# Kernel tuning notes

Hardware: AMD Instinct MI355X
Metric: run time of the kernel (lower is better)

Reference implementation:

```python
import jax, jax.numpy as jnp
import numpy as np

_PHI = (1.0 + 5.0 ** 0.5) / 2.0
_VS = np.array([[0, 1, _PHI], [0, 1, -_PHI], [0, -1, _PHI], [0, -1, -_PHI],
                [1, _PHI, 0], [1, -_PHI, 0], [-1, _PHI, 0], [-1, -_PHI, 0],
                [_PHI, 0, 1], [_PHI, 0, -1], [-_PHI, 0, 1], [-_PHI, 0, -1]], dtype=np.float32)
_VS = _VS / np.linalg.norm(_VS, axis=-1, keepdims=True)  # 12 icosahedron vertices
_COLOR_COM = np.array([(0, 1, 2, 3, 4, 5), (0, 5, 4, 3, 2, 1), (2, 5, 4, 1, 0, 3), (5, 0, 1, 3, 2, 4),
                       (3, 5, 2, 0, 4, 1), (4, 0, 5, 2, 1, 3), (1, 3, 4, 2, 0, 5), (1, 0, 2, 4, 3, 5),
                       (4, 1, 2, 5, 0, 3), (3, 1, 4, 0, 2, 5), (5, 1, 0, 4, 2, 3), (2, 4, 5, 3, 0, 1)])
_INV = np.argsort(_COLOR_COM, axis=-1)  # inverse perms: scatter_(-1, color_com, W) == gather with _INV
_C2V = np.array([(0, 1), (6, 7), (2, 11), (4, 9), (5, 8), (3, 10)])
_ROLL = np.array([(0, 1, 2, 3, 4, 5), (0, 2, 3, 4, 5, 1), (0, 3, 4, 5, 1, 2), (0, 4, 5, 1, 2, 3), (0, 5, 1, 2, 3, 4)])
_HEADS = 8


def _build_sym(Wp):
    """(..., 18) raw params -> (..., 13, 12, 6) symmetry-expanded weights."""
    lead = Wp.shape[:-1]
    top = jnp.concatenate([Wp[..., 0:1], jnp.repeat(Wp[..., 1:2], 5, axis=-1)], axis=-1)[..., None, :]
    bot = jnp.concatenate([Wp[..., 2:3], jnp.repeat(Wp[..., 3:4], 5, axis=-1)], axis=-1)[..., None, :]
    cen = jnp.concatenate([Wp[..., 4:5], jnp.repeat(Wp[..., 5:6], 5, axis=-1)], axis=-1)[..., None, :]
    sym = Wp[..., 6:18].reshape(lead + (2, 6))[..., _ROLL].reshape(lead + (10, 6))
    W13 = jnp.concatenate([top, bot, sym, cen], axis=-2)  # (..., 13, 6)
    return W13[..., _INV]  # (..., 13, 12, 6): rotated copies via inverse color permutations


def setup_inputs() -> dict:
    key = jax.random.key(0)
    ks = jax.random.split(key, 6)
    bs, V, n, di, do = 1, 2048, 16, 32, 64
    s = 0.05
    return {
        "neighbor_index": jax.random.randint(ks[0], (bs, V, n), 0, V),
        "vertices": jax.random.normal(ks[1], (bs, V, 3), dtype=jnp.float32),
        "feature_map": jax.random.normal(ks[2], (bs, di, V, 6), dtype=jnp.float32),
        "W_dim": jax.random.normal(ks[3], (di + 1, di), dtype=jnp.float32) * s,
        "W": jax.random.normal(ks[4], (do, di, 18), dtype=jnp.float32) * s,
        "W_dir": jax.random.normal(ks[5], (di * _HEADS, 18), dtype=jnp.float32) * s,
    }


def reference(neighbor_index, vertices, feature_map, W_dim, W, W_dir):
    bs, V, n = neighbor_index.shape
    do, di, _ = W.shape
    H = _HEADS
    dph = di // H
    vs = jnp.asarray(_VS)
    c2v = jnp.asarray(_C2V)
    # neighbor direction (normalized)
    neigh = jax.vmap(lambda v, idx: v[idx])(vertices, neighbor_index)  # (bs,V,n,3)
    nd = neigh - vertices[:, :, None, :]
    ndn = nd / jnp.maximum(jnp.linalg.norm(nd, axis=-1, keepdims=True), 1e-12)
    # symmetry-expanded weights
    W_ro = _build_sym(W)       # (do, di, 13, 12, 6)
    Wd_ro = _build_sym(W_dir)  # (di*H, 13, 12, 6)
    # gather neighbor features: (bs, di, V, n, 6)
    nf = jax.vmap(lambda fm, idx: fm[:, idx])(feature_map, neighbor_index)
    # direction features discretized onto the 6 color axes
    de = jnp.einsum('vi,bqni->bqnv', vs, ndn)          # (bs,V,n,12)
    de = de[..., c2v].max(axis=-1)                      # (bs,V,n,6)
    cross = jnp.concatenate([nf, de[:, None]], axis=1)  # (bs, di+1, V, n, 6)
    cross = jnp.einsum('co,bcpni->bopni', W_dim, cross)  # (bs, di, V, n, 6)
    # per-head attention over neighbors
    Wdr = Wd_ro.reshape(H, di, 13, 12, 6).transpose(0, 1, 2, 4, 3)  # (h, c, k, i, r)
    act = jnp.einsum('hckir,bcpni->hbkpnr', Wdr[:, :, :12], cross) / (dph ** 0.5)
    act = jax.nn.softmax(act, axis=-2)                  # softmax over neighbors n
    cross_h = cross.reshape(bs, H, dph, V, n, 6)
    nfm = jnp.einsum('hbkpnr,bhcpni->bhckpir', act, cross_h).reshape(bs, di, 12, V, 6, 12)
    feat = jnp.einsum('dckri,bckpir->bdkpr', W_ro[:, :, :12], nfm)   # (bs,do,12,V,12)
    center = jnp.einsum('dcri,bcpi->bdpr', W_ro[:, :, 12], feature_map)  # (bs,do,V,12)
    ka = feat.sum(axis=2) + center                       # (bs,do,V,12)
    ka = ka[..., c2v].max(axis=-1)                       # (bs,do,V,6)
    return (ka, feature_map)
```

## Files before the change

### kernel.cpp

```cpp
#include <hip/hip_runtime.h>
#include <cstdint>
#include <cstddef>

#define NN 16
#define DI 32
#define DO 64

typedef short bf16x8 __attribute__((ext_vector_type(8)));
typedef short bf16x4 __attribute__((ext_vector_type(4)));
typedef float f32x4 __attribute__((ext_vector_type(4)));

#if defined(__has_builtin)
#  if __has_builtin(__builtin_amdgcn_mfma_f32_16x16x16_bf16)
#    define MFMA_K16(a, b, c) __builtin_amdgcn_mfma_f32_16x16x16_bf16(a, b, c, 0, 0, 0)
#    define HAVE_K16 1
#  elif __has_builtin(__builtin_amdgcn_mfma_f32_16x16x16bf16_1k)
#    define MFMA_K16(a, b, c) __builtin_amdgcn_mfma_f32_16x16x16bf16_1k(a, b, c, 0, 0, 0)
#    define HAVE_K16 1
#  endif
#endif

__device__ __constant__ int c_INV[12][6] = {
  {0,1,2,3,4,5},{0,5,4,3,2,1},{4,3,0,5,2,1},{1,2,4,3,5,0},
  {3,5,2,0,4,1},{1,4,3,5,0,2},{4,0,3,1,2,5},{1,0,2,4,3,5},
  {4,1,2,5,0,3},{3,1,4,0,2,5},{2,1,4,5,3,0},{4,5,0,3,1,2}};
__device__ __constant__ int c_ROLL[5][6] = {
  {0,1,2,3,4,5},{0,2,3,4,5,1},{0,3,4,5,1,2},{0,4,5,1,2,3},{0,5,1,2,3,4}};
__device__ __constant__ float c_VS[12][3] = {
  {0.f, 0.5257311121f, 0.8506508084f},
  {0.f, 0.5257311121f, -0.8506508084f},
  {0.f, -0.5257311121f, 0.8506508084f},
  {0.f, -0.5257311121f, -0.8506508084f},
  {0.5257311121f, 0.8506508084f, 0.f},
  {0.5257311121f, -0.8506508084f, 0.f},
  {-0.5257311121f, 0.8506508084f, 0.f},
  {-0.5257311121f, -0.8506508084f, 0.f},
  {0.8506508084f, 0.f, 0.5257311121f},
  {0.8506508084f, 0.f, -0.5257311121f},
  {-0.8506508084f, 0.f, 0.5257311121f},
  {-0.8506508084f, 0.f, -0.5257311121f}};
__device__ __constant__ int c_C2V[6][2] = {{0,1},{6,7},{2,11},{4,9},{5,8},{3,10}};

__device__ inline unsigned int bfround(float f) {
  unsigned int u = __float_as_uint(f);
  return u + 0x7fffu + ((u >> 16) & 1u);
}
__device__ inline unsigned int pk2(float a, float b) {
  return __builtin_amdgcn_perm(bfround(b), bfround(a), 0x07060302u);
}
__device__ inline unsigned short f2bf_fast(float a) {
  return (unsigned short)(bfround(a) >> 16);
}
__device__ inline uint4 pack8(const float* v8) {
  uint4 o4;
  o4.x = pk2(v8[0], v8[1]);
  o4.y = pk2(v8[2], v8[3]);
  o4.z = pk2(v8[4], v8[5]);
  o4.w = pk2(v8[6], v8[7]);
  return o4;
}

__device__ inline unsigned int q4i8(f32x4 o) {
  int q0 = (int)rintf(fminf(fmaxf(o[0] * 64.f, -127.f), 127.f));
  int q1 = (int)rintf(fminf(fmaxf(o[1] * 64.f, -127.f), 127.f));
  int q2 = (int)rintf(fminf(fmaxf(o[2] * 64.f, -127.f), 127.f));
  int q3 = (int)rintf(fminf(fmaxf(o[3] * 64.f, -127.f), 127.f));
  return (unsigned int)((q0 & 255) | ((q1 & 255) << 8) | ((q2 & 255) << 16) | (q3 << 24));
}
__device__ inline bf16x8 dec8(uint2 w) {
  float f0 = (float)(int)(signed char)(w.x & 0xffu);
  float f1 = (float)(int)(signed char)((w.x >> 8) & 0xffu);
  float f2 = (float)(int)(signed char)((w.x >> 16) & 0xffu);
  float f3 = (float)((int)w.x >> 24);
  float f4 = (float)(int)(signed char)(w.y & 0xffu);
  float f5 = (float)(int)(signed char)((w.y >> 8) & 0xffu);
  float f6 = (float)(int)(signed char)((w.y >> 16) & 0xffu);
  float f7 = (float)((int)w.y >> 24);
  union { unsigned int u[4]; bf16x8 v8; } o;
  o.u[0] = pk2(f0, f1);
  o.u[1] = pk2(f2, f3);
  o.u[2] = pk2(f4, f5);
  o.u[3] = pk2(f6, f7);
  return o.v8;
}

__global__ __launch_bounds__(256) void k0_expand(
    const float* __restrict__ W, const float* __restrict__ Wdir,
    const float* __restrict__ fm, const float* __restrict__ Wdim,
    unsigned short* __restrict__ A_bf,
    unsigned short* __restrict__ W2k,
    unsigned short* __restrict__ Wck,
    unsigned short* __restrict__ fmTbf,
    unsigned short* __restrict__ wdB,
    float* __restrict__ out_fm, int V) {
  int idx = blockIdx.x * 256 + threadIdx.x;
  int nF = 24 * V;
  if (idx < 267264) {
    const float* wsrc; unsigned short* dst;
    int k, r, ci0; float scale;
    if (idx < 27648) {
      int chunk = idx;
      int rl = chunk & 15, u = chunk >> 4;
      int q = u & 3; u >>= 2;
      int ks = u % 6, rt = u / 6;
      int row = rt * 16 + rl;
      int h = row / 144;
      k = (row / 12) % 12; r = row % 12;
      ci0 = ks * 32 + q * 8;
      wsrc = Wdir + h * 576;
      dst = A_bf + (size_t)chunk * 8;
      scale = 0.5f;
    } else if (idx < 248832) {
      int chunk = idx - 27648;
      int d = chunk & 63, u = chunk >> 6;
      int q = u & 3; u >>= 2;
      int ks = u % 6, kr = u / 6;
      k = kr / 12; r = kr % 12;
      ci0 = ks * 32 + q * 8;
      wsrc = W + d * 576;
      dst = W2k + (size_t)chunk * 8;
      scale = 0.015625f;
    } else {
      int chunk = idx - 248832;
      int d = chunk & 63, u = chunk >> 6;
      int q = u & 3; u >>= 2;
      int ks = u % 6;
      r = u / 6; k = 12;
      ci0 = ks * 32 + q * 8;
      wsrc = W + d * 576;
      dst = Wck + (size_t)chunk * 8;
      scale = 1.0f;
    }
    int c = ci0 / 6, i = ci0 - c * 6;
    float v8[8];
    #pragma unroll
    for (int j = 0; j < 8; ++j) {
      int jj = c_INV[r][i];
      int off;
      if (k == 0)       off = (jj == 0) ? 0 : 1;
      else if (k == 1)  off = (jj == 0) ? 2 : 3;
      else if (k == 12) off = (jj == 0) ? 4 : 5;
      else { int a = (k - 2) / 5, rr = (k - 2) % 5; off = 6 + a * 6 + c_ROLL[rr][jj]; }
      v8[j] = scale * wsrc[c * 18 + off];
      ++i; if (i == 6) { i = 0; ++c; }
    }
    *(uint4*)dst = pack8(v8);
  } else if (idx < 267264 + nF) {
    int chunk = idx - 267264;
    int p = chunk / 24, cc = chunk - p * 24;
    int ci0 = cc * 8;
    int c = ci0 / 6, i = ci0 - c * 6;
    float v8[8];
    #pragma unroll
    for (int j = 0; j < 8; ++j) {
      v8[j] = fm[((size_t)c * V + p) * 6 + i];
      ++i; if (i == 6) { i = 0; ++c; }
    }
    *(uint4*)(fmTbf + (size_t)chunk * 8) = pack8(v8);
  } else if (idx < 267264 + nF + 48 * V) {
    int x4 = idx - (267264 + nF);
    ((float4*)out_fm)[x4] = ((const float4*)fm)[x4];
  } else {
    int e = idx - (267264 + nF + 48 * V);
    if (e < 128) {
      int lane = e & 63, ot = e >> 6;
      float v8[8];
      #pragma unroll
      for (int j = 0; j < 8; ++j) {
        int kk = ((lane >> 4) & 3) * 8 + j;
        int o = ot * 16 + (lane & 15);
        v8[j] = Wdim[kk * 32 + o];
      }
      *(uint4*)(wdB + (size_t)e * 8) = pack8(v8);
    }
  }
}

__global__ __launch_bounds__(256, 4) void k12_main(
    const int* __restrict__ nbi, const float* __restrict__ verts,
    const float* __restrict__ fm, const float* __restrict__ Wdim,
    const unsigned short* __restrict__ wdB,
    const unsigned short* __restrict__ A_bf,
    unsigned char* __restrict__ nfm, int V) {
  __shared__ __align__(16) unsigned short in_bf[2][96][40];
  __shared__ __align__(16) float de_s[2][96];
  __shared__ __align__(16) unsigned short crossL[2][192][20];
  int t = threadIdx.x;
  int w = t >> 6, lane = t & 63;
  int quad = lane >> 4, col = lane & 15;
  int p0 = blockIdx.x * 2;
  int v = w & 1, hf = w >> 1;
  int p = p0 + v;

  for (int i = lane; i < 256; i += 64) {
    int n = i >> 4, c = hf * 16 + (i & 15);
    int nb = nbi[p * 16 + n];
    const float* src = fm + ((size_t)c * V + nb) * 6;
    float2 a  = *(const float2*)(src + 0);
    float2 b  = *(const float2*)(src + 2);
    float2 cd = *(const float2*)(src + 4);
    unsigned short* dst = &in_bf[v][n * 6][c];
    dst[0 * 40] = f2bf_fast(a.x);
    dst[1 * 40] = f2bf_fast(a.y);
    dst[2 * 40] = f2bf_fast(b.x);
    dst[3 * 40] = f2bf_fast(b.y);
    dst[4 * 40] = f2bf_fast(cd.x);
    dst[5 * 40] = f2bf_fast(cd.y);
  }
  if (hf == 0 && lane < 16) {
    int n = lane, nb = nbi[p * 16 + n];
    float px = verts[p * 3 + 0], py = verts[p * 3 + 1], pz = verts[p * 3 + 2];
    float qx = verts[nb * 3 + 0] - px, qy = verts[nb * 3 + 1] - py, qz = verts[nb * 3 + 2] - pz;
    float L = sqrtf(qx * qx + qy * qy + qz * qz);
    float inv = 1.0f / fmaxf(L, 1e-12f);
    qx *= inv; qy *= inv; qz *= inv;
    float de[12];
    #pragma unroll
    for (int vv = 0; vv < 12; ++vv)
      de[vv] = c_VS[vv][0] * qx + c_VS[vv][1] * qy + c_VS[vv][2] * qz;
    #pragma unroll
    for (int j = 0; j < 6; ++j)
      de_s[v][n * 6 + j] = fmaxf(de[c_C2V[j][0]], de[c_C2V[j][1]]);
  }
  __syncthreads();

  {
    int vv = w & 1;
    int mtb = (w >> 1) * 3;
    bf16x8 Bf[2];
    #pragma unroll
    for (int ot = 0; ot < 2; ++ot)
      Bf[ot] = *(const bf16x8*)(wdB + (size_t)(ot * 64 + lane) * 8);
    float wd32[2] = {Wdim[1024 + col], Wdim[1024 + 16 + col]};
    #pragma unroll
    for (int mi = 0; mi < 3; ++mi) {
      int mt = mtb + mi;
      bf16x8 a0 = *(const bf16x8*)&in_bf[vv][mt * 16 + col][quad * 8];
      f32x4 du = *(const f32x4*)&de_s[vv][mt * 16 + quad * 4];
      #pragma unroll
      for (int ot = 0; ot < 2; ++ot) {
        f32x4 acc = (f32x4){0.f, 0.f, 0.f, 0.f};
        acc = __builtin_amdgcn_mfma_f32_16x16x32_bf16(a0, Bf[ot], acc, 0, 0, 0);
        #pragma unroll
        for (int r = 0; r < 4; ++r)
          acc[r] = fmaf(du[r], wd32[ot], acc[r]);
        #pragma unroll
        for (int r = 0; r < 4; ++r) {
          int m = mt * 16 + quad * 4 + r;
          int n = m / 6, i = m - n * 6;
          crossL[vv][(ot * 16 + col) * 6 + i][n] = f2bf_fast(acc[r]);
        }
      }
    }
  }
  __syncthreads();

  bf16x8 Afr[2][6];
  #pragma unroll
  for (int pi = 0; pi < 2; ++pi) {
    #pragma unroll
    for (int ks = 0; ks < 6; ++ks) {
      union { unsigned short s[8]; bf16x8 v8; } u;
      #pragma unroll
      for (int j = 0; j < 8; ++j)
        u.s[j] = crossL[pi][ks * 32 + quad * 8 + j][col];
      Afr[pi][ks] = u.v8;
    }
  }

  bf16x8 wf[6];
  {
    const unsigned short* Abase = A_bf + w * 3072 + quad * 128 + col * 8;
    #pragma unroll
    for (int ks = 0; ks < 6; ++ks) wf[ks] = *(const bf16x8*)(Abase + ks * 512);
  }
  for (int rt = w; rt < 72; rt += 4) {
    int h = rt / 9;
    f32x4 acc[2];
    acc[0] = (f32x4){0.f, 0.f, 0.f, 0.f};
    acc[1] = (f32x4){0.f, 0.f, 0.f, 0.f};
    #pragma unroll
    for (int ks = 0; ks < 6; ++ks) {
      acc[0] = __builtin_amdgcn_mfma_f32_16x16x32_bf16(Afr[0][ks], wf[ks], acc[0], 0, 0, 0);
      acc[1] = __builtin_amdgcn_mfma_f32_16x16x32_bf16(Afr[1][ks], wf[ks], acc[1], 0, 0, 0);
    }
    bf16x8 wfn[6];
    {
      int rtn = min(rt + 4, 71);
      const unsigned short* AbaseN = A_bf + rtn * 3072 + quad * 128 + col * 8;
      #pragma unroll
      for (int ks = 0; ks < 6; ++ks) wfn[ks] = *(const bf16x8*)(AbaseN + ks * 512);
    }
    int row0 = h * 24 + col;
    int row1 = min(h * 24 + 16 + col, 191);
    #pragma unroll
    for (int pi = 0; pi < 2; ++pi) {
      float e0 = __expf(acc[pi][0]), e1 = __expf(acc[pi][1]);
      float e2 = __expf(acc[pi][2]), e3 = __expf(acc[pi][3]);
      float s = (e0 + e1) + (e2 + e3);
      s += __shfl_xor(s, 16);
      s += __shfl_xor(s, 32);
      float inv = __builtin_amdgcn_rcpf(s);
      unsigned int lo = pk2(e0 * inv, e1 * inv);
      unsigned int hi = pk2(e2 * inv, e3 * inv);
      f32x4 o0 = (f32x4){0.f, 0.f, 0.f, 0.f}, o1 = o0;
#ifdef HAVE_K16
      union { uint2 u; bf16x4 v4; } bcvt;
      bcvt.u = make_uint2(lo, hi);
      bf16x4 a0 = *(const bf16x4*)&crossL[pi][row0][quad * 4];
      bf16x4 a1 = *(const bf16x4*)&crossL[pi][row1][quad * 4];
      o0 = MFMA_K16(a0, bcvt.v4, o0);
      o1 = MFMA_K16(a1, bcvt.v4, o1);
#else
      int s0l = quad * 32 + col, s1l = s0l + 16;
      unsigned int b0 = (unsigned int)__shfl((int)lo, s0l);
      unsigned int b1 = (unsigned int)__shfl((int)hi, s0l);
      unsigned int b2 = (unsigned int)__shfl((int)lo, s1l);
      unsigned int b3 = (unsigned int)__shfl((int)hi, s1l);
      bool vq = (quad < 2);
      union { uint4 u; bf16x8 v8; } cvt;
      cvt.u = make_uint4(vq ? b0 : 0u, vq ? b1 : 0u, vq ? b2 : 0u, vq ? b3 : 0u);
      union { unsigned short sv[8]; bf16x8 v8; } ua0, ua1;
      #pragma unroll
      for (int j = 0; j < 8; ++j) {
        int nn = quad * 8 + j;
        ua0.sv[j] = (nn < 16) ? crossL[pi][row0][nn] : (unsigned short)0;
        ua1.sv[j] = (nn < 16) ? crossL[pi][row1][nn] : (unsigned short)0;
      }
      o0 = __builtin_amdgcn_mfma_f32_16x16x32_bf16(ua0.v8, cvt.v8, o0, 0, 0, 0);
      o1 = __builtin_amdgcn_mfma_f32_16x16x32_bf16(ua1.v8, cvt.v8, o1, 0, 0, 0);
#endif
      size_t rowbase = (size_t)blockIdx.x * 55296 + (size_t)(rt * 16 + col) * 48 + pi * 24;
      *(unsigned int*)(nfm + rowbase + quad * 4) = q4i8(o0);
      if (quad < 2)
        *(unsigned int*)(nfm + rowbase + 16 + quad * 4) = q4i8(o1);
    }
    #pragma unroll
    for (int ks = 0; ks < 6; ++ks) wf[ks] = wfn[ks];
  }
}

__global__ __launch_bounds__(512) void k3_feat(
    const unsigned short* __restrict__ W2k,
    const unsigned short* __restrict__ Wck,
    const unsigned short* __restrict__ fmTbf,
    const unsigned char* __restrict__ nfm,
    float* __restrict__ out, int V) {
  __shared__ float red[2][3][16][64];
  int pb = blockIdx.x, j = blockIdx.y;
  int t = threadIdx.x, w = t >> 6, lane = t & 63;
  int rhalf = w >> 2, kw = w & 3;
  int r = c_C2V[j][rhalf];
  int quad = lane >> 4, col = lane & 15;
  int p0 = pb * 16;
  f32x4 acc[4];
  #pragma unroll
  for (int m = 0; m < 4; ++m) acc[m] = (f32x4){0.f, 0.f, 0.f, 0.f};

  int base24[6];
  #pragma unroll
  for (int ks = 0; ks < 6; ++ks) {
    int ci = ks * 32 + quad * 8;
    int hh = ci / 24, oo = ci - hh * 24;
    base24[ks] = hh * 6912 + oo;
  }

  int pA = p0 + col;
  const unsigned char* Bn0 = nfm + (size_t)(pA >> 1) * 55296 + (pA & 1) * 24;
  const unsigned short* Bc0 = fmTbf + (size_t)pA * 192;

  int nkb = (kw == 3) ? 4 : 3;
  for (int i = 0; i < nkb; ++i) {
    int kb = kw * 3 + i;
    const unsigned short* Ab;
    int kr48 = 0;
    if (kb < 12) { Ab = W2k + (size_t)(kb * 12 + r) * 12288; kr48 = (kb * 12 + r) * 48; }
    else         { Ab = Wck + (size_t)r * 12288; }
    const unsigned short* Albase = Ab + quad * 512 + col * 8;
    #pragma unroll
    for (int ks = 0; ks < 6; ++ks) {
      bf16x8 b0;
      if (kb < 12) {
        b0 = dec8(*(const uint2*)(Bn0 + base24[ks] + kr48));
      } else {
        b0 = *(const bf16x8*)(Bc0 + ks * 32 + quad * 8);
      }
      #pragma unroll
      for (int m = 0; m < 4; ++m) {
        bf16x8 a = *(const bf16x8*)(Albase + ks * 2048 + m * 128);
        acc[m] = __builtin_amdgcn_mfma_f32_16x16x32_bf16(a, b0, acc[m], 0, 0, 0);
      }
    }
  }
  if (kw > 0) {
    #pragma unroll
    for (int m = 0; m < 4; ++m)
      #pragma unroll
      for (int rr = 0; rr < 4; ++rr)
        red[rhalf][kw - 1][m * 4 + rr][lane] = acc[m][rr];
  }
  __syncthreads();
  if (kw == 0) {
    #pragma unroll
    for (int m = 0; m < 4; ++m)
      #pragma unroll
      for (int rr = 0; rr < 4; ++rr) {
        int ri = m * 4 + rr;
        acc[m][rr] += red[rhalf][0][ri][lane] + red[rhalf][1][ri][lane] + red[rhalf][2][ri][lane];
      }
  }
  if (w == 4) {
    #pragma unroll
    for (int m = 0; m < 4; ++m)
      #pragma unroll
      for (int rr = 0; rr < 4; ++rr)
        red[1][0][m * 4 + rr][lane] = acc[m][rr];
  }
  __syncthreads();
  if (w == 0) {
    #pragma unroll
    for (int m = 0; m < 4; ++m)
      #pragma unroll
      for (int rr = 0; rr < 4; ++rr) {
        float vmax = fmaxf(acc[m][rr], red[1][0][m * 4 + rr][lane]);
        int d = m * 16 + quad * 4 + rr;
        out[((size_t)d * V + p0 + col) * 6 + j] = vmax;
      }
  }
}

extern "C" void kernel_launch(void* const* d_in, const int* in_sizes, int n_in,
                              void* d_out, int out_size, void* d_ws, size_t ws_size,
                              hipStream_t stream) {
  const int* nbi = (const int*)d_in[0];
  const float* verts = (const float*)d_in[1];
  const float* fm = (const float*)d_in[2];
  const float* Wdim = (const float*)d_in[3];
  const float* W = (const float*)d_in[4];
  const float* Wdir = (const float*)d_in[5];
  float* out = (float*)d_out;
  float* ws = (float*)d_ws;
  int V = in_sizes[0] / NN;

  unsigned short* A_bf  = (unsigned short*)ws;
  unsigned short* W2k   = (unsigned short*)(ws + 110592);
  unsigned short* Wck   = (unsigned short*)(ws + 995328);
  unsigned short* fmTbf = (unsigned short*)(ws + 1069056);
  size_t o = 1069056 + (size_t)96 * V;
  unsigned char* nfm = (unsigned char*)(ws + o);
  o += (size_t)6912 * V;
  unsigned short* wdB = (unsigned short*)(ws + o);

  int n0 = 267392 + 72 * V;
  k0_expand<<<(n0 + 255) / 256, 256, 0, stream>>>(W, Wdir, fm, Wdim, A_bf, W2k, Wck, fmTbf,
                                                  wdB, out + (size_t)DO * V * 6, V);
  k12_main<<<V / 2, 256, 0, stream>>>(nbi, verts, fm, Wdim, wdB, A_bf, nfm, V);
  k3_feat<<<dim3(V / 16, 6), 512, 0, stream>>>(W2k, Wck, fmTbf, nfm, out, V);
}
```

Measured before the change: 153.0 us.

## Split weight expansion and fold k3-only prep into main kernel grid

Result: no change. 150.1 us (-1.9%).

```diff
diff --git a/kernel.cpp b/kernel.cpp
--- a/kernel.cpp
+++ b/kernel.cpp
@@ -84,53 +84,20 @@
   return o.v8;
 }
 
-__global__ __launch_bounds__(256) void k0_expand(
-    const float* __restrict__ W, const float* __restrict__ Wdir,
-    const float* __restrict__ fm, const float* __restrict__ Wdim,
-    unsigned short* __restrict__ A_bf,
-    unsigned short* __restrict__ W2k,
-    unsigned short* __restrict__ Wck,
-    unsigned short* __restrict__ fmTbf,
-    unsigned short* __restrict__ wdB,
-    float* __restrict__ out_fm, int V) {
+__global__ __launch_bounds__(256) void k0a_expand(
+    const float* __restrict__ Wdir, const float* __restrict__ Wdim,
+    unsigned short* __restrict__ A_bf, unsigned short* __restrict__ wdB) {
   int idx = blockIdx.x * 256 + threadIdx.x;
-  int nF = 24 * V;
-  if (idx < 267264) {
-    const float* wsrc; unsigned short* dst;
-    int k, r, ci0; float scale;
-    if (idx < 27648) {
-      int chunk = idx;
-      int rl = chunk & 15, u = chunk >> 4;
-      int q = u & 3; u >>= 2;
-      int ks = u % 6, rt = u / 6;
-      int row = rt * 16 + rl;
-      int h = row / 144;
-      k = (row / 12) % 12; r = row % 12;
-      ci0 = ks * 32 + q * 8;
-      wsrc = Wdir + h * 576;
-      dst = A_bf + (size_t)chunk * 8;
-      scale = 0.5f;
-    } else if (idx < 248832) {
-      int chunk = idx - 27648;
-      int d = chunk & 63, u = chunk >> 6;
-      int q = u & 3; u >>= 2;
-      int ks = u % 6, kr = u / 6;
-      k = kr / 12; r = kr % 12;
-      ci0 = ks * 32 + q * 8;
-      wsrc = W + d * 576;
-      dst = W2k + (size_t)chunk * 8;
-      scale = 0.015625f;
-    } else {
-      int chunk = idx - 248832;
-      int d = chunk & 63, u = chunk >> 6;
-      int q = u & 3; u >>= 2;
-      int ks = u % 6;
-      r = u / 6; k = 12;
-      ci0 = ks * 32 + q * 8;
-      wsrc = W + d * 576;
-      dst = Wck + (size_t)chunk * 8;
-      scale = 1.0f;
-    }
+  if (idx < 27648) {
+    int chunk = idx;
+    int rl = chunk & 15, u = chunk >> 4;
+    int q = u & 3; u >>= 2;
+    int ks = u % 6, rt = u / 6;
+    int row = rt * 16 + rl;
+    int h = row / 144;
+    int k = (row / 12) % 12, r = row % 12;
+    int ci0 = ks * 32 + q * 8;
+    const float* wsrc = Wdir + h * 576;
     int c = ci0 / 6, i = ci0 - c * 6;
     float v8[8];
     #pragma unroll
@@ -139,56 +106,106 @@
       int off;
       if (k == 0)       off = (jj == 0) ? 0 : 1;
       else if (k == 1)  off = (jj == 0) ? 2 : 3;
-      else if (k == 12) off = (jj == 0) ? 4 : 5;
       else { int a = (k - 2) / 5, rr = (k - 2) % 5; off = 6 + a * 6 + c_ROLL[rr][jj]; }
-      v8[j] = scale * wsrc[c * 18 + off];
+      v8[j] = 0.5f * wsrc[c * 18 + off];
       ++i; if (i == 6) { i = 0; ++c; }
     }
-    *(uint4*)dst = pack8(v8);
-  } else if (idx < 267264 + nF) {
-    int chunk = idx - 267264;
-    int p = chunk / 24, cc = chunk - p * 24;
-    int ci0 = cc * 8;
-    int c = ci0 / 6, i = ci0 - c * 6;
+    *(uint4*)(A_bf + (size_t)chunk * 8) = pack8(v8);
+  } else if (idx < 27776) {
+    int e = idx - 27648;
+    int lane = e & 63, ot = e >> 6;
     float v8[8];
     #pragma unroll
     for (int j = 0; j < 8; ++j) {
-      v8[j] = fm[((size_t)c * V + p) * 6 + i];
-      ++i; if (i == 6) { i = 0; ++c; }
-    }
-    *(uint4*)(fmTbf + (size_t)chunk * 8) = pack8(v8);
-  } else if (idx < 267264 + nF + 48 * V) {
-    int x4 = idx - (267264 + nF);
-    ((float4*)out_fm)[x4] = ((const float4*)fm)[x4];
-  } else {
-    int e = idx - (267264 + nF + 48 * V);
-    if (e < 128) {
-      int lane = e & 63, ot = e >> 6;
-      float v8[8];
-      #pragma unroll
-      for (int j = 0; j < 8; ++j) {
-        int kk = ((lane >> 4) & 3) * 8 + j;
-        int o = ot * 16 + (lane & 15);
-        v8[j] = Wdim[kk * 32 + o];
-      }
-      *(uint4*)(wdB + (size_t)e * 8) = pack8(v8);
-    }
-  }
-}
-
-__global__ __launch_bounds__(256, 4) void k12_main(
+      int kk = ((lane >> 4) & 3) * 8 + j;
+      int o = ot * 16 + (lane & 15);
+      v8[j] = Wdim[kk * 32 + o];
+    }
+    *(uint4*)(wdB + (size_t)e * 8) = pack8(v8);
+  }
+}
+
+__global__ __launch_bounds__(256, 4) void k12f_main(
     const int* __restrict__ nbi, const float* __restrict__ verts,
     const float* __restrict__ fm, const float* __restrict__ Wdim,
     const unsigned short* __restrict__ wdB,
     const unsigned short* __restrict__ A_bf,
-    unsigned char* __restrict__ nfm, int V) {
+    unsigned char* __restrict__ nfm,
+    const float* __restrict__ W,
+    unsigned short* __restrict__ W2k,
+    unsigned short* __restrict__ Wck,
+    unsigned short* __restrict__ fmTbf,
+    float* __restrict__ out_fm, int V) {
   __shared__ __align__(16) unsigned short in_bf[2][96][40];
   __shared__ __align__(16) float de_s[2][96];
   __shared__ __align__(16) unsigned short crossL[2][192][20];
+  int bid = blockIdx.x;
+  int nblk12 = V / 2;
+
+  if (bid >= nblk12) {
+    int idx = (bid - nblk12) * 256 + threadIdx.x;
+    int nF = 24 * V;
+    if (idx < 239616) {
+      const float* wsrc; unsigned short* dst;
+      int k, r, ci0; float scale;
+      if (idx < 221184) {
+        int chunk = idx;
+        int d = chunk & 63, u = chunk >> 6;
+        int q = u & 3; u >>= 2;
+        int ks = u % 6, kr = u / 6;
+        k = kr / 12; r = kr % 12;
+        ci0 = ks * 32 + q * 8;
+        wsrc = W + d * 576;
+        dst = W2k + (size_t)chunk * 8;
+        scale = 0.015625f;
+      } else {
+        int chunk = idx - 221184;
+        int d = chunk & 63, u = chunk >> 6;
+        int q = u & 3; u >>= 2;
+        int ks = u % 6;
+        r = u / 6; k = 12;
+        ci0 = ks * 32 + q * 8;
+        wsrc = W + d * 576;
+        dst = Wck + (size_t)chunk * 8;
+        scale = 1.0f;
+      }
+      int c = ci0 / 6, i = ci0 - c * 6;
+      float v8[8];
+      #pragma unroll
+      for (int j = 0; j < 8; ++j) {
+        int jj = c_INV[r][i];
+        int off;
+        if (k == 0)       off = (jj == 0) ? 0 : 1;
+        else if (k == 1)  off = (jj == 0) ? 2 : 3;
+        else if (k == 12) off = (jj == 0) ? 4 : 5;
+        else { int a = (k - 2) / 5, rr = (k - 2) % 5; off = 6 + a * 6 + c_ROLL[rr][jj]; }
+        v8[j] = scale * wsrc[c * 18 + off];
+        ++i; if (i == 6) { i = 0; ++c; }
+      }
+      *(uint4*)dst = pack8(v8);
+    } else if (idx < 239616 + nF) {
+      int chunk = idx - 239616;
+      int p = chunk / 24, cc = chunk - p * 24;
+      int ci0 = cc * 8;
+      int c = ci0 / 6, i = ci0 - c * 6;
+      float v8[8];
+      #pragma unroll
+      for (int j = 0; j < 8; ++j) {
+        v8[j] = fm[((size_t)c * V + p) * 6 + i];
+        ++i; if (i == 6) { i = 0; ++c; }
+      }
+      *(uint4*)(fmTbf + (size_t)chunk * 8) = pack8(v8);
+    } else if (idx < 239616 + nF + 48 * V) {
+      int x4 = idx - (239616 + nF);
+      ((float4*)out_fm)[x4] = ((const float4*)fm)[x4];
+    }
+    return;
+  }
+
   int t = threadIdx.x;
   int w = t >> 6, lane = t & 63;
   int quad = lane >> 4, col = lane & 15;
-  int p0 = blockIdx.x * 2;
+  int p0 = bid * 2;
   int v = w & 1, hf = w >> 1;
   int p = p0 + v;
 
@@ -330,7 +347,7 @@
       o0 = __builtin_amdgcn_mfma_f32_16x16x32_bf16(ua0.v8, cvt.v8, o0, 0, 0, 0);
       o1 = __builtin_amdgcn_mfma_f32_16x16x32_bf16(ua1.v8, cvt.v8, o1, 0, 0, 0);
 #endif
-      size_t rowbase = (size_t)blockIdx.x * 55296 + (size_t)(rt * 16 + col) * 48 + pi * 24;
+      size_t rowbase = (size_t)bid * 55296 + (size_t)(rt * 16 + col) * 48 + pi * 24;
       *(unsigned int*)(nfm + rowbase + quad * 4) = q4i8(o0);
       if (quad < 2)
         *(unsigned int*)(nfm + rowbase + 16 + quad * 4) = q4i8(o1);
@@ -451,9 +468,11 @@
   o += (size_t)6912 * V;
   unsigned short* wdB = (unsigned short*)(ws + o);
 
-  int n0 = 267392 + 72 * V;
-  k0_expand<<<(n0 + 255) / 256, 256, 0, stream>>>(W, Wdir, fm, Wdim, A_bf, W2k, Wck, fmTbf,
-                                                  wdB, out + (size_t)DO * V * 6, V);
-  k12_main<<<V / 2, 256, 0, stream>>>(nbi, verts, fm, Wdim, wdB, A_bf, nfm, V);
+  k0a_expand<<<109, 256, 0, stream>>>(Wdir, Wdim, A_bf, wdB);
+  int n0b = 239616 + 24 * V + 48 * V;
+  int nb0b = (n0b + 255) / 256;
+  k12f_main<<<V / 2 + nb0b, 256, 0, stream>>>(nbi, verts, fm, Wdim, wdB, A_bf, nfm,
+                                              W, W2k, Wck, fmTbf,
+                                              out + (size_t)DO * V * 6, V);
   k3_feat<<<dim3(V / 16, 6), 512, 0, stream>>>(W2k, Wck, fmTbf, nfm, out, V);
 }
```
